# Kernel optimization log

Measured on AMD Instinct MI355X. Metric: run time of the kernel, lower is better.

Reference implementation:

```python
import jax, jax.numpy as jnp
import numpy as np

N_PEP, N_MHC, N_TCR = 20000, 5000, 100000
EMB, HID = 128, 256
E_PM, E_MT = 200000, 400000
B = 50000


def setup_inputs() -> dict:
    key = jax.random.key(0)
    ks = jax.random.split(key, 30)
    f32 = jnp.float32

    def w(k, shape, fan_in):
        # torch Linear default: U(-1/sqrt(fan_in), 1/sqrt(fan_in))
        lim = 1.0 / np.sqrt(fan_in)
        return jax.random.uniform(k, shape, dtype=f32, minval=-lim, maxval=lim)

    inp = {
        # embedding tables (learned params)
        "emb_pep": jax.random.normal(ks[0], (N_PEP, EMB), dtype=f32),
        "emb_mhc": jax.random.normal(ks[1], (N_MHC, EMB), dtype=f32),
        "emb_tcr": jax.random.normal(ks[2], (N_TCR, EMB), dtype=f32),
        # edge lists (src=edge_index[0], dst=edge_index[1])
        "src_pm": jax.random.randint(ks[3], (E_PM,), 0, N_PEP, dtype=jnp.int32),
        "dst_pm": jax.random.randint(ks[4], (E_PM,), 0, N_MHC, dtype=jnp.int32),
        "src_mt": jax.random.randint(ks[5], (E_MT,), 0, N_MHC, dtype=jnp.int32),
        "dst_mt": jax.random.randint(ks[6], (E_MT,), 0, N_TCR, dtype=jnp.int32),
        # triplet pack indices
        "pack_pep": jax.random.randint(ks[7], (B,), 0, N_PEP, dtype=jnp.int32),
        "pack_mhc": jax.random.randint(ks[8], (B,), 0, N_MHC, dtype=jnp.int32),
        "pack_tcr": jax.random.randint(ks[9], (B,), 0, N_TCR, dtype=jnp.int32),
        # SAGEConv params: Wl (aggregated neighbors, with bias), Wr (root, no bias)
        # layer 1: pep->mhc (src 128, dst 128); mhc->tcr (src 128, dst 128)
        "l1_pm_Wl": w(ks[10], (HID, EMB), EMB), "l1_pm_bl": w(ks[11], (HID,), EMB),
        "l1_pm_Wr": w(ks[12], (HID, EMB), EMB),
        "l1_mt_Wl": w(ks[13], (HID, EMB), EMB), "l1_mt_bl": w(ks[14], (HID,), EMB),
        "l1_mt_Wr": w(ks[15], (HID, EMB), EMB),
        # layer 2: pep->mhc (src 128, dst 256); mhc->tcr (src 256, dst 256)
        "l2_pm_Wl": w(ks[16], (HID, EMB), EMB), "l2_pm_bl": w(ks[17], (HID,), EMB),
        "l2_pm_Wr": w(ks[18], (HID, HID), HID),
        "l2_mt_Wl": w(ks[19], (HID, HID), HID), "l2_mt_bl": w(ks[20], (HID,), HID),
        "l2_mt_Wr": w(ks[21], (HID, HID), HID),
        # proj_pep and head MLP
        "proj_W": w(ks[22], (HID, EMB), EMB), "proj_b": w(ks[23], (HID,), EMB),
        "head_W1": w(ks[24], (HID, 3 * HID), 3 * HID), "head_b1": w(ks[25], (HID,), 3 * HID),
        "head_W2": w(ks[26], (1, HID), HID), "head_b2": w(ks[27], (1,), HID),
    }
    return inp


def _sage(x_src, x_dst, src, dst, Wl, bl, Wr, n_dst):
    # SAGEConv(mean): lin_l(mean_{j in N(i)} x_src[j]) + lin_r(x_dst[i])
    msg = jax.ops.segment_sum(x_src[src], dst, num_segments=n_dst)  # [n_dst, d_src]
    cnt = jax.ops.segment_sum(jnp.ones((src.shape[0],), x_src.dtype), dst, num_segments=n_dst)
    mean = msg / jnp.maximum(cnt, 1.0)[:, None]
    return mean @ Wl.T + bl + x_dst @ Wr.T


def reference(emb_pep, emb_mhc, emb_tcr,
              src_pm, dst_pm, src_mt, dst_mt,
              pack_pep, pack_mhc, pack_tcr,
              l1_pm_Wl, l1_pm_bl, l1_pm_Wr, l1_mt_Wl, l1_mt_bl, l1_mt_Wr,
              l2_pm_Wl, l2_pm_bl, l2_pm_Wr, l2_mt_Wl, l2_mt_bl, l2_mt_Wr,
              proj_W, proj_b, head_W1, head_b1, head_W2, head_b2):
    relu = jax.nn.relu
    # layer 1 (HeteroConv reads all relations from the same input dict)
    mhc1 = relu(_sage(emb_pep, emb_mhc, src_pm, dst_pm, l1_pm_Wl, l1_pm_bl, l1_pm_Wr, N_MHC))
    tcr1 = relu(_sage(emb_mhc, emb_tcr, src_mt, dst_mt, l1_mt_Wl, l1_mt_bl, l1_mt_Wr, N_TCR))
    # layer 2 ('pep' is never a destination, so it keeps its embedding)
    mhc2 = relu(_sage(emb_pep, mhc1, src_pm, dst_pm, l2_pm_Wl, l2_pm_bl, l2_pm_Wr, N_MHC))
    tcr2 = relu(_sage(mhc1, tcr1, src_mt, dst_mt, l2_mt_Wl, l2_mt_bl, l2_mt_Wr, N_TCR))
    # projections + triplet gather (dropout disabled: inference)
    hp = (emb_pep @ proj_W.T + proj_b)[pack_pep]  # [B, HID]
    hm = mhc2[pack_mhc]
    ht = tcr2[pack_tcr]
    z = jnp.concatenate([hp, hm, ht], axis=-1)  # [B, 3*HID]
    hidden = relu(z @ head_W1.T + head_b1)
    logits = hidden @ head_W2.T + head_b2
    return logits.squeeze(-1)
```

## Files before the change

kernel.cpp:

```cpp
#include <hip/hip_runtime.h>

constexpr int NPEP = 20000, NMHC = 5000, NTCR = 100000;
constexpr int EPM = 200000, EMT = 400000, BB = 50000;
constexpr int MAXU = 50000;

typedef __attribute__((ext_vector_type(8))) short bf16x8;
typedef __attribute__((ext_vector_type(4))) float f32x4;

__device__ inline ushort f2bf(float x) {
    union { float f; unsigned u; } v; v.f = x;
    unsigned r = (v.u + 0x7FFF + ((v.u >> 16) & 1)) >> 16;
    return (ushort)r;
}
__device__ inline float bf2f(ushort b) {
    union { unsigned u; float f; } t; t.u = ((unsigned)b) << 16; return t.f;
}
__device__ inline void bf2x2(unsigned u, float& a, float& b) {
    union { unsigned x; float f; } t1, t2;
    t1.x = u << 16; t2.x = u & 0xffff0000u;
    a = t1.f; b = t2.f;
}
__device__ inline ushort4 f4bf(float4 v) {
    return make_ushort4(f2bf(v.x), f2bf(v.y), f2bf(v.z), f2bf(v.w));
}

__global__ __launch_bounds__(256) void prep_kernel(
    int* __restrict__ ibz,
    const float4* __restrict__ emb_pep, ushort4* __restrict__ emb_pep_b,
    const float4* __restrict__ Wr1f, ushort4* __restrict__ Wr1_b,
    const float4* __restrict__ Wr2f, ushort4* __restrict__ Wr2_b,
    const float* __restrict__ head_W1, ushort4* __restrict__ W1b_b, ushort4* __restrict__ W1c_b,
    const float* __restrict__ l1_pm_Wl, const float* __restrict__ l1_pm_Wr,
    const float* __restrict__ l1_mt_Wl, ushort* __restrict__ Wcat1_b,
    const float* __restrict__ l2_pm_Wl, const float* __restrict__ l2_pm_Wr,
    const float* __restrict__ l2_mt_Wl, ushort* __restrict__ Wcat2_b,
    const float4* __restrict__ emb_mhc, ushort* __restrict__ Acat1,
    const float* __restrict__ proj_W, const float* __restrict__ proj_b,
    ushort* __restrict__ Wcomp_b, float* __restrict__ bp) {
    __shared__ float red[128];
    const int b = blockIdx.x, tid = threadIdx.x;
    if (b < 303) {
        int i = b * 256 + tid;
        if (i < 77500) ((int4*)ibz)[i] = make_int4(0, 0, 0, 0);
    } else if (b < 2803) {
        int i = (b - 303) * 256 + tid;
        if (i < 640000) emb_pep_b[i] = f4bf(emb_pep[i]);
    } else if (b < 2835) {
        int i = (b - 2803) * 256 + tid;
        if (i < 8192) Wr1_b[i] = f4bf(Wr1f[i]);
    } else if (b < 2899) {
        int i = (b - 2835) * 256 + tid;
        if (i < 16384) Wr2_b[i] = f4bf(Wr2f[i]);
    } else if (b < 2963) {
        int i = (b - 2899) * 256 + tid;
        if (i < 16384) {
            int n = i >> 6, k4 = (i & 63) * 4;
            float4 v = *(const float4*)(head_W1 + (size_t)n * 768 + 256 + k4);
            W1b_b[i] = f4bf(v);
        }
    } else if (b < 3027) {
        int i = (b - 2963) * 256 + tid;
        if (i < 16384) {
            int n = i >> 6, k4 = (i & 63) * 4;
            float4 v = *(const float4*)(head_W1 + (size_t)n * 768 + 512 + k4);
            W1c_b[i] = f4bf(v);
        }
    } else if (b < 3539) {
        int idx = (b - 3027) * 256 + tid;
        if (idx < 131072) {
            int r = idx >> 8, k = idx & 255;
            float v;
            if (r < 256) v = (k < 128) ? l1_pm_Wl[r * 128 + k] : l1_pm_Wr[r * 128 + (k - 128)];
            else         v = (k < 128) ? 0.f : l1_mt_Wl[(r - 256) * 128 + (k - 128)];
            Wcat1_b[idx] = f2bf(v);
        }
    } else if (b < 4307) {
        int idx = (b - 3539) * 256 + tid;
        if (idx < 196608) {
            int r = idx / 384, k = idx - r * 384;
            float v;
            if (r < 256) v = (k < 128) ? l2_pm_Wl[r * 128 + k] : l2_pm_Wr[r * 256 + (k - 128)];
            else         v = (k < 128) ? 0.f : l2_mt_Wl[(r - 256) * 256 + (k - 128)];
            Wcat2_b[idx] = f2bf(v);
        }
    } else if (b < 4932) {
        int i4 = (b - 4307) * 256 + tid;
        if (i4 < 160000) {
            int r = i4 >> 5, c4 = (i4 & 31) * 4;
            *(ushort4*)(Acat1 + (size_t)r * 256 + 128 + c4) = f4bf(emb_mhc[i4]);
        }
    } else {
        int i = b - 4932;
        const float* w1row = head_W1 + (size_t)i * 768;
        if (tid < 128) {
            float acc = 0.f;
            for (int k = 0; k < 256; k++) acc += w1row[k] * proj_W[k * 128 + tid];
            Wcomp_b[i * 128 + tid] = f2bf(acc);
            float pb = w1row[2 * tid] * proj_b[2 * tid] + w1row[2 * tid + 1] * proj_b[2 * tid + 1];
            red[tid] = pb;
        }
        __syncthreads();
        if (tid < 64) { red[tid] += red[tid + 64]; }
        __syncthreads();
        if (tid < 32) { red[tid] += red[tid + 32]; }
        __syncthreads();
        if (tid == 0) {
            float s = 0.f;
            for (int j = 0; j < 32; j++) s += red[j];
            bp[i] = s;
        }
    }
}

__global__ void hist2_kernel(const int* __restrict__ dst_pm, const int* __restrict__ dst_mt,
                             const int* __restrict__ pack_tcr,
                             int* __restrict__ deg_pm, int* __restrict__ deg_mt,
                             int* __restrict__ mark) {
    int t = blockIdx.x * blockDim.x + threadIdx.x;
    if (t < EPM) atomicAdd(&deg_pm[dst_pm[t]], 1);
    else if (t < EPM + EMT) atomicAdd(&deg_mt[dst_mt[t - EPM]], 1);
    else if (t < EPM + EMT + BB) mark[pack_tcr[t - EPM - EMT]] = 1;
}

__global__ __launch_bounds__(256) void blocksum2_kernel(const int* __restrict__ deg_pm,
                                                        const int* __restrict__ deg_mt,
                                                        const int* __restrict__ mark,
                                                        int* __restrict__ bsum_pm,
                                                        int* __restrict__ bsum_mt,
                                                        int* __restrict__ bsum_mk) {
    __shared__ int red[256];
    const int tid = threadIdx.x;
    const int* deg; int n, bi; int* bsum;
    if (blockIdx.x < 5) { deg = deg_pm; n = NMHC; bi = blockIdx.x; bsum = bsum_pm; }
    else if (blockIdx.x < 103) { deg = deg_mt; n = NTCR; bi = blockIdx.x - 5; bsum = bsum_mt; }
    else { deg = mark; n = NTCR; bi = blockIdx.x - 103; bsum = bsum_mk; }
    const int base = bi * 1024;
    int s = 0;
#pragma unroll
    for (int j = 0; j < 4; j++) {
        int i = base + tid + j * 256;
        if (i < n) s += deg[i];
    }
    red[tid] = s;
    __syncthreads();
    for (int off = 128; off > 0; off >>= 1) {
        if (tid < off) red[tid] += red[tid + off];
        __syncthreads();
    }
    if (tid == 0) bsum[bi] = red[0];
}

__global__ __launch_bounds__(128) void scanb2_kernel(int* __restrict__ bsum_pm,
                                                     int* __restrict__ bsum_mt,
                                                     int* __restrict__ bsum_mk) {
    __shared__ int s[128];
    const int tid = threadIdx.x;
    int* bsum = (blockIdx.x == 0) ? bsum_pm : ((blockIdx.x == 1) ? bsum_mt : bsum_mk);
    const int nb = (blockIdx.x == 0) ? 5 : 98;
    int v = (tid < nb) ? bsum[tid] : 0;
    s[tid] = v;
    __syncthreads();
    for (int off = 1; off < 128; off <<= 1) {
        int t = (tid >= off) ? s[tid - off] : 0;
        __syncthreads();
        s[tid] += t;
        __syncthreads();
    }
    if (tid < nb) bsum[tid] = (tid > 0) ? s[tid - 1] : 0;
    if (tid == 0) bsum[nb] = s[nb - 1];
}

__global__ __launch_bounds__(256) void emit2_kernel(const int* __restrict__ deg_pm,
                                                    const int* __restrict__ deg_mt,
                                                    const int* __restrict__ mark,
                                                    const int* __restrict__ bsum_pm,
                                                    const int* __restrict__ bsum_mt,
                                                    const int* __restrict__ bsum_mk,
                                                    int* __restrict__ rp_pm, float* __restrict__ cnt_pm,
                                                    int* __restrict__ rp_mt, float* __restrict__ cnt_mt,
                                                    int* __restrict__ list) {
    __shared__ int tsum[256];
    const int tid = threadIdx.x;
    const int* deg; const int* bsum; int* rp; float* cnt; int n, nb, bi, mode;
    if (blockIdx.x < 5) { deg = deg_pm; bsum = bsum_pm; rp = rp_pm; cnt = cnt_pm; n = NMHC; nb = 5; bi = blockIdx.x; mode = 0; }
    else if (blockIdx.x < 103) { deg = deg_mt; bsum = bsum_mt; rp = rp_mt; cnt = cnt_mt; n = NTCR; nb = 98; bi = blockIdx.x - 5; mode = 0; }
    else { deg = mark; bsum = bsum_mk; rp = nullptr; cnt = nullptr; n = NTCR; nb = 98; bi = blockIdx.x - 103; mode = 1; }
    const int i0 = bi * 1024 + tid * 4;
    int4 v = make_int4(0, 0, 0, 0);
    if (i0 + 3 < n) v = *(const int4*)(deg + i0);
    else if (i0 < n) {
        int t[4] = {0, 0, 0, 0};
        for (int j = 0; j < 4 && i0 + j < n; j++) t[j] = deg[i0 + j];
        v = make_int4(t[0], t[1], t[2], t[3]);
    }
    int s = v.x + v.y + v.z + v.w;
    tsum[tid] = s;
    __syncthreads();
    for (int off = 1; off < 256; off <<= 1) {
        int t = (tid >= off) ? tsum[tid - off] : 0;
        __syncthreads();
        tsum[tid] += t;
        __syncthreads();
    }
    int ex = ((tid > 0) ? tsum[tid - 1] : 0) + bsum[bi];
    if (mode == 0) {
        if (i0 + 3 < n) {
            int r1 = ex + v.x, r2 = r1 + v.y, r3 = r2 + v.z;
            *(int4*)(rp + i0) = make_int4(ex, r1, r2, r3);
            *(float4*)(cnt + i0) = make_float4((float)v.x, (float)v.y, (float)v.z, (float)v.w);
        } else if (i0 < n) {
            int r = ex;
            int vv[4] = {v.x, v.y, v.z, v.w};
            for (int j = 0; j < 4 && i0 + j < n; j++) {
                rp[i0 + j] = r;
                cnt[i0 + j] = (float)vv[j];
                r += vv[j];
            }
        }
        if (bi == 0 && tid == 0) rp[n] = bsum[nb];
    } else {
        int p = ex;
        int vv[4] = {v.x, v.y, v.z, v.w};
#pragma unroll
        for (int j = 0; j < 4; j++) {
            if (i0 + j < n && vv[j]) list[p++] = i0 + j;
        }
    }
}

__global__ void fill2_kernel(const int* __restrict__ src_pm, const int* __restrict__ dst_pm,
                             const int* __restrict__ src_mt, const int* __restrict__ dst_mt,
                             const int* __restrict__ rp_pm, int* __restrict__ cur_pm, int* __restrict__ csr_pm,
                             const int* __restrict__ rp_mt, int* __restrict__ cur_mt, int* __restrict__ csr_mt) {
    int t = blockIdx.x * blockDim.x + threadIdx.x;
    if (t < EPM) {
        int d = dst_pm[t];
        int pos = atomicAdd(&cur_pm[d], 1);
        csr_pm[rp_pm[d] + pos] = src_pm[t];
    } else if (t < EPM + EMT) {
        int t2 = t - EPM;
        int d = dst_mt[t2];
        int pos = atomicAdd(&cur_mt[d], 1);
        csr_mt[rp_mt[d] + pos] = src_mt[t2];
    }
}

__global__ __launch_bounds__(256) void gatherpm_kernel(const int* __restrict__ rp,
                                                       const int* __restrict__ csr_src,
                                                       const float* __restrict__ X,
                                                       ushort* __restrict__ A1, ushort* __restrict__ A2,
                                                       int n) {
    const int tid = threadIdx.x;
    const int r = blockIdx.x * 8 + (tid >> 5);
    const int lane = tid & 31;
    if (r >= n) return;
    const int e0 = rp[r], e1 = rp[r + 1];
    float4 s = make_float4(0.f, 0.f, 0.f, 0.f);
    for (int e = e0; e < e1; e++) {
        const int sidx = csr_src[e];
        float4 v = ((const float4*)(X + (long)sidx * 128))[lane];
        s.x += v.x; s.y += v.y; s.z += v.z; s.w += v.w;
    }
    float sc = 1.f / fmaxf((float)(e1 - e0), 1.f);
    ushort4 o = make_ushort4(f2bf(s.x * sc), f2bf(s.y * sc), f2bf(s.z * sc), f2bf(s.w * sc));
    *(ushort4*)(A1 + (size_t)r * 256 + lane * 4) = o;
    *(ushort4*)(A2 + (size_t)r * 384 + lane * 4) = o;
}

__global__ __launch_bounds__(256) void gatherb2_kernel(const int* __restrict__ rp,
                                                       const int* __restrict__ csr_src,
                                                       const ushort* __restrict__ Z1,
                                                       const ushort* __restrict__ Z2,
                                                       const int* __restrict__ list,
                                                       const int* __restrict__ nrowsp,
                                                       const float4* __restrict__ etc4,
                                                       ushort4* __restrict__ etc_bc,
                                                       float* __restrict__ cntc,
                                                       ushort* __restrict__ a1,
                                                       ushort* __restrict__ a2) {
    const int tid = threadIdx.x;
    const int r = blockIdx.x * 8 + (tid >> 5);
    const int lane = tid & 31;
    const int nrows = nrowsp[0];
    if (r >= nrows) return;
    const int orig = list[r];
    const int e0 = rp[orig], e1 = rp[orig + 1];
    float4 ev = etc4[(size_t)orig * 32 + lane];
    etc_bc[(size_t)r * 32 + lane] = f4bf(ev);
    if (lane == 0) cntc[r] = (float)(e1 - e0);
    float s1[8] = {}, s2[8] = {};
    for (int e = e0; e < e1; e++) {
        const int sidx = csr_src[e];
        uint4 u1 = *(const uint4*)(Z1 + (size_t)sidx * 256 + lane * 8);
        uint4 u2 = *(const uint4*)(Z2 + (size_t)sidx * 256 + lane * 8);
        float a, b;
        bf2x2(u1.x, a, b); s1[0] += a; s1[1] += b;
        bf2x2(u1.y, a, b); s1[2] += a; s1[3] += b;
        bf2x2(u1.z, a, b); s1[4] += a; s1[5] += b;
        bf2x2(u1.w, a, b); s1[6] += a; s1[7] += b;
        bf2x2(u2.x, a, b); s2[0] += a; s2[1] += b;
        bf2x2(u2.y, a, b); s2[2] += a; s2[3] += b;
        bf2x2(u2.z, a, b); s2[4] += a; s2[5] += b;
        bf2x2(u2.w, a, b); s2[6] += a; s2[7] += b;
    }
    uint4 w1, w2;
    w1.x = (unsigned)f2bf(s1[0]) | ((unsigned)f2bf(s1[1]) << 16);
    w1.y = (unsigned)f2bf(s1[2]) | ((unsigned)f2bf(s1[3]) << 16);
    w1.z = (unsigned)f2bf(s1[4]) | ((unsigned)f2bf(s1[5]) << 16);
    w1.w = (unsigned)f2bf(s1[6]) | ((unsigned)f2bf(s1[7]) << 16);
    w2.x = (unsigned)f2bf(s2[0]) | ((unsigned)f2bf(s2[1]) << 16);
    w2.y = (unsigned)f2bf(s2[2]) | ((unsigned)f2bf(s2[3]) << 16);
    w2.z = (unsigned)f2bf(s2[4]) | ((unsigned)f2bf(s2[5]) << 16);
    w2.w = (unsigned)f2bf(s2[6]) | ((unsigned)f2bf(s2[7]) << 16);
    *(uint4*)(a1 + (size_t)r * 256 + lane * 8) = w1;
    *(uint4*)(a2 + (size_t)r * 256 + lane * 8) = w2;
}

template <int K, int NB0, bool RELU0, bool G2>
__global__ __launch_bounds__(256, 2) void mfma_fused_kernel(
    int M, const ushort* __restrict__ A, const ushort* __restrict__ W,
    const float* __restrict__ bias,
    ushort* __restrict__ out0, int s0, ushort* __restrict__ out1) {
    constexpr int RS = 40;
    __shared__ ushort Als[128 * RS];
    __shared__ ushort Wls[128 * RS];
    const int tid = threadIdx.x;
    const int m0 = blockIdx.x * 128, n0 = blockIdx.y * 128;
    const int lane = tid & 63, w = tid >> 6;
    const int wm = w >> 1, wn = w & 1;
    const int m16 = lane & 15, q = lane >> 4;

    f32x4 acc[4][4] = {};

    for (int k0 = 0; k0 < K; k0 += 32) {
        bf16x8 a_st[2], w_st[2];
#pragma unroll
        for (int r = 0; r < 2; r++) {
            int chunk = tid + r * 256;
            int row = chunk >> 2, off = (chunk & 3) * 8;
            int ga = min(m0 + row, M - 1);
            a_st[r] = *(const bf16x8*)(A + (size_t)ga * K + k0 + off);
            w_st[r] = *(const bf16x8*)(W + (size_t)(n0 + row) * K + k0 + off);
        }
        __syncthreads();
#pragma unroll
        for (int r = 0; r < 2; r++) {
            int chunk = tid + r * 256;
            int row = chunk >> 2, off = (chunk & 3) * 8;
            *(bf16x8*)(&Als[row * RS + off]) = a_st[r];
            *(bf16x8*)(&Wls[row * RS + off]) = w_st[r];
        }
        __syncthreads();
        bf16x8 af[4], bf[4];
#pragma unroll
        for (int t = 0; t < 4; t++) {
            af[t] = *(const bf16x8*)(&Als[(wm * 64 + t * 16 + m16) * RS + q * 8]);
            bf[t] = *(const bf16x8*)(&Wls[(wn * 64 + t * 16 + m16) * RS + q * 8]);
        }
#pragma unroll
        for (int mt = 0; mt < 4; mt++)
#pragma unroll
            for (int nt = 0; nt < 4; nt++)
                acc[mt][nt] = __builtin_amdgcn_mfma_f32_16x16x32_bf16(af[mt], bf[nt], acc[mt][nt], 0, 0, 0);
    }

    const bool g1 = G2 && ((int)blockIdx.y >= NB0);
#pragma unroll
    for (int mt = 0; mt < 4; mt++) {
#pragma unroll
        for (int i = 0; i < 4; i++) {
            int row = m0 + wm * 64 + mt * 16 + q * 4 + i;
            if (row >= M) continue;
#pragma unroll
            for (int nt = 0; nt < 4; nt++) {
                int col = n0 + wn * 64 + nt * 16 + m16;
                float v = acc[mt][nt][i];
                if (!g1) {
                    v += bias[col];
                    if (RELU0) v = fmaxf(v, 0.f);
                    out0[(size_t)row * s0 + col] = f2bf(v);
                } else {
                    out1[(size_t)row * 256 + (col - NB0 * 128)] = f2bf(v);
                }
            }
        }
    }
}

template <int K>
__global__ __launch_bounds__(256, 2) void rowgemm_kernel(
    const int* __restrict__ nrowsp, const ushort* __restrict__ A, const ushort* __restrict__ W,
    const float* __restrict__ bias, const float* __restrict__ cnt,
    const ushort* __restrict__ accp, ushort* __restrict__ Cb) {
    constexpr int RS = 40;
    __shared__ ushort Als[128 * RS];
    __shared__ ushort Wls[256 * RS];
    const int tid = threadIdx.x;
    const int M = nrowsp[0];
    const int m0 = blockIdx.x * 128;
    if (m0 >= M) return;
    const int lane = tid & 63, w = tid >> 6;
    const int wm = w >> 1, wn = w & 1;
    const int m16 = lane & 15, q = lane >> 4;

    f32x4 acc[4][8] = {};

    for (int k0 = 0; k0 < K; k0 += 32) {
        bf16x8 a_st[2], w_st[4];
#pragma unroll
        for (int r = 0; r < 2; r++) {
            int chunk = tid + r * 256;
            int row = chunk >> 2, off = (chunk & 3) * 8;
            int ga = min(m0 + row, M - 1);
            a_st[r] = *(const bf16x8*)(A + (size_t)ga * K + k0 + off);
        }
#pragma unroll
        for (int r = 0; r < 4; r++) {
            int chunk = tid + r * 256;
            int row = chunk >> 2, off = (chunk & 3) * 8;
            w_st[r] = *(const bf16x8*)(W + (size_t)row * K + k0 + off);
        }
        __syncthreads();
#pragma unroll
        for (int r = 0; r < 2; r++) {
            int chunk = tid + r * 256;
            int row = chunk >> 2, off = (chunk & 3) * 8;
            *(bf16x8*)(&Als[row * RS + off]) = a_st[r];
        }
#pragma unroll
        for (int r = 0; r < 4; r++) {
            int chunk = tid + r * 256;
            int row = chunk >> 2, off = (chunk & 3) * 8;
            *(bf16x8*)(&Wls[row * RS + off]) = w_st[r];
        }
        __syncthreads();
        bf16x8 af[4], bf[8];
#pragma unroll
        for (int t = 0; t < 4; t++)
            af[t] = *(const bf16x8*)(&Als[(wm * 64 + t * 16 + m16) * RS + q * 8]);
#pragma unroll
        for (int t = 0; t < 8; t++)
            bf[t] = *(const bf16x8*)(&Wls[(wn * 128 + t * 16 + m16) * RS + q * 8]);
#pragma unroll
        for (int mt = 0; mt < 4; mt++)
#pragma unroll
            for (int nt = 0; nt < 8; nt++)
                acc[mt][nt] = __builtin_amdgcn_mfma_f32_16x16x32_bf16(af[mt], bf[nt], acc[mt][nt], 0, 0, 0);
    }

#pragma unroll
    for (int mt = 0; mt < 4; mt++) {
#pragma unroll
        for (int i = 0; i < 4; i++) {
            int row = m0 + wm * 64 + mt * 16 + q * 4 + i;
            if (row >= M) continue;
            float es = 1.f / fmaxf(cnt[row], 1.f);
#pragma unroll
            for (int nt = 0; nt < 8; nt++) {
                int col = wn * 128 + nt * 16 + m16;
                float v = acc[mt][nt][i] + bias[col] + bf2f(accp[(size_t)row * 256 + col]) * es;
                Cb[(size_t)row * 256 + col] = f2bf(fmaxf(v, 0.f));
            }
        }
    }
}

__global__ __launch_bounds__(256, 2) void tcr2ht_kernel(
    const int* __restrict__ nrowsp, const int* __restrict__ list,
    const ushort* __restrict__ T1, const ushort* __restrict__ Wr2,
    const ushort* __restrict__ W1c,
    const float* __restrict__ bl2, const float* __restrict__ cnt,
    const ushort* __restrict__ acc2, ushort* __restrict__ Ht) {
    constexpr int RS = 40;
    constexpr int RS2 = 264;
    __shared__ ushort Als[64 * RS];
    __shared__ ushort Wls[256 * RS];
    __shared__ ushort T[64 * RS2];
    const int tid = threadIdx.x;
    const int M = nrowsp[0];
    const int m0 = blockIdx.x * 64;
    if (m0 >= M) return;
    const int lane = tid & 63, w = tid >> 6;
    const int m16 = lane & 15, q = lane >> 4;

    {
        f32x4 acc[4][4] = {};
        for (int k0 = 0; k0 < 256; k0 += 32) {
            bf16x8 a_st, w_st[4];
            {
                int row = tid >> 2, off = (tid & 3) * 8;
                int ga = min(m0 + row, M - 1);
                a_st = *(const bf16x8*)(T1 + (size_t)ga * 256 + k0 + off);
            }
#pragma unroll
            for (int r = 0; r < 4; r++) {
                int chunk = tid + r * 256;
                int row = chunk >> 2, off = (chunk & 3) * 8;
                w_st[r] = *(const bf16x8*)(Wr2 + (size_t)row * 256 + k0 + off);
            }
            __syncthreads();
            {
                int row = tid >> 2, off = (tid & 3) * 8;
                *(bf16x8*)(&Als[row * RS + off]) = a_st;
            }
#pragma unroll
            for (int r = 0; r < 4; r++) {
                int chunk = tid + r * 256;
                int row = chunk >> 2, off = (chunk & 3) * 8;
                *(bf16x8*)(&Wls[row * RS + off]) = w_st[r];
            }
            __syncthreads();
            bf16x8 af[4], bf[4];
#pragma unroll
            for (int t = 0; t < 4; t++) {
                af[t] = *(const bf16x8*)(&Als[(t * 16 + m16) * RS + q * 8]);
                bf[t] = *(const bf16x8*)(&Wls[(w * 64 + t * 16 + m16) * RS + q * 8]);
            }
#pragma unroll
            for (int mt = 0; mt < 4; mt++)
#pragma unroll
                for (int nt = 0; nt < 4; nt++)
                    acc[mt][nt] = __builtin_amdgcn_mfma_f32_16x16x32_bf16(af[mt], bf[nt], acc[mt][nt], 0, 0, 0);
        }
#pragma unroll
        for (int mt = 0; mt < 4; mt++)
#pragma unroll
            for (int i = 0; i < 4; i++) {
                int lr = mt * 16 + q * 4 + i;
                int rc = min(m0 + lr, M - 1);
                float es = 1.f / fmaxf(cnt[rc], 1.f);
#pragma unroll
                for (int nt = 0; nt < 4; nt++) {
                    int col = w * 64 + nt * 16 + m16;
                    float v = acc[mt][nt][i] + bl2[col] + bf2f(acc2[(size_t)rc * 256 + col]) * es;
                    T[lr * RS2 + col] = f2bf(fmaxf(v, 0.f));
                }
            }
    }
    __syncthreads();

    {
        f32x4 acc[4][4] = {};
        for (int k0 = 0; k0 < 256; k0 += 32) {
            bf16x8 af[4], bf[4];
#pragma unroll
            for (int t = 0; t < 4; t++)
                af[t] = *(const bf16x8*)(&T[(t * 16 + m16) * RS2 + k0 + q * 8]);
#pragma unroll
            for (int t = 0; t < 4; t++) {
                int n = w * 64 + t * 16 + m16;
                bf[t] = *(const bf16x8*)(W1c + (size_t)n * 256 + k0 + q * 8);
            }
#pragma unroll
            for (int mt = 0; mt < 4; mt++)
#pragma unroll
                for (int nt = 0; nt < 4; nt++)
                    acc[mt][nt] = __builtin_amdgcn_mfma_f32_16x16x32_bf16(af[mt], bf[nt], acc[mt][nt], 0, 0, 0);
        }
#pragma unroll
        for (int mt = 0; mt < 4; mt++)
#pragma unroll
            for (int i = 0; i < 4; i++) {
                int row = m0 + mt * 16 + q * 4 + i;
                if (row >= M) continue;
                int orig = list[row];
#pragma unroll
                for (int nt = 0; nt < 4; nt++) {
                    int col = w * 64 + nt * 16 + m16;
                    Ht[(size_t)orig * 256 + col] = f2bf(acc[mt][nt][i]);
                }
            }
    }
}

template <int K, bool HASB>
__global__ __launch_bounds__(256, 2) void mfma_out_kernel(
    int M, const ushort* __restrict__ A, const ushort* __restrict__ W,
    const float* __restrict__ bias, ushort* __restrict__ out) {
    constexpr int RS = 40;
    __shared__ ushort Als[128 * RS];
    __shared__ ushort Wls[128 * RS];
    const int tid = threadIdx.x;
    const int m0 = blockIdx.x * 128, n0 = blockIdx.y * 128;
    const int lane = tid & 63, w = tid >> 6;
    const int wm = w >> 1, wn = w & 1;
    const int m16 = lane & 15, q = lane >> 4;

    f32x4 acc[4][4] = {};

    for (int k0 = 0; k0 < K; k0 += 32) {
        bf16x8 a_st[2], w_st[2];
#pragma unroll
        for (int r = 0; r < 2; r++) {
            int chunk = tid + r * 256;
            int row = chunk >> 2, off = (chunk & 3) * 8;
            int ga = min(m0 + row, M - 1);
            a_st[r] = *(const bf16x8*)(A + (size_t)ga * K + k0 + off);
            w_st[r] = *(const bf16x8*)(W + (size_t)(n0 + row) * K + k0 + off);
        }
        __syncthreads();
#pragma unroll
        for (int r = 0; r < 2; r++) {
            int chunk = tid + r * 256;
            int row = chunk >> 2, off = (chunk & 3) * 8;
            *(bf16x8*)(&Als[row * RS + off]) = a_st[r];
            *(bf16x8*)(&Wls[row * RS + off]) = w_st[r];
        }
        __syncthreads();
        bf16x8 af[4], bf[4];
#pragma unroll
        for (int t = 0; t < 4; t++) {
            af[t] = *(const bf16x8*)(&Als[(wm * 64 + t * 16 + m16) * RS + q * 8]);
            bf[t] = *(const bf16x8*)(&Wls[(wn * 64 + t * 16 + m16) * RS + q * 8]);
        }
#pragma unroll
        for (int mt = 0; mt < 4; mt++)
#pragma unroll
            for (int nt = 0; nt < 4; nt++)
                acc[mt][nt] = __builtin_amdgcn_mfma_f32_16x16x32_bf16(af[mt], bf[nt], acc[mt][nt], 0, 0, 0);
    }

#pragma unroll
    for (int mt = 0; mt < 4; mt++) {
#pragma unroll
        for (int i = 0; i < 4; i++) {
            int row = m0 + wm * 64 + mt * 16 + q * 4 + i;
            if (row >= M) continue;
#pragma unroll
            for (int nt = 0; nt < 4; nt++) {
                int col = n0 + wn * 64 + nt * 16 + m16;
                float v = acc[mt][nt][i];
                if (HASB) v += bias[col];
                out[(size_t)row * 256 + col] = f2bf(v);
            }
        }
    }
}

__global__ __launch_bounds__(256) void combine_kernel(
    const ushort* __restrict__ Hp, const ushort* __restrict__ Hm, const ushort* __restrict__ Ht,
    const int* __restrict__ pp, const int* __restrict__ pm, const int* __restrict__ pt,
    const float* __restrict__ b1, const float* __restrict__ W2, const float* __restrict__ b2,
    float* __restrict__ out) {
    const int tid = threadIdx.x;
    const int lane = tid & 63, w = tid >> 6;
    const int c = lane * 4;
    const float4 b1v = *(const float4*)(b1 + c);
    const float4 w2v = *(const float4*)(W2 + c);
    const float b2v = b2[0];
    const int base = blockIdx.x * 32 + w * 8;
#pragma unroll
    for (int t = 0; t < 8; t++) {
        int i = base + t;
        if (i >= BB) return;
        int ra = pp[i], rb = pm[i], rc = pt[i];
        ushort4 ua = *(const ushort4*)(Hp + (size_t)ra * 256 + c);
        ushort4 ub = *(const ushort4*)(Hm + (size_t)rb * 256 + c);
        ushort4 uc = *(const ushort4*)(Ht + (size_t)rc * 256 + c);
        float h0 = fmaxf(bf2f(ua.x) + bf2f(ub.x) + bf2f(uc.x) + b1v.x, 0.f);
        float h1 = fmaxf(bf2f(ua.y) + bf2f(ub.y) + bf2f(uc.y) + b1v.y, 0.f);
        float h2 = fmaxf(bf2f(ua.z) + bf2f(ub.z) + bf2f(uc.z) + b1v.z, 0.f);
        float h3 = fmaxf(bf2f(ua.w) + bf2f(ub.w) + bf2f(uc.w) + b1v.w, 0.f);
        float p = h0 * w2v.x + h1 * w2v.y + h2 * w2v.z + h3 * w2v.w;
#pragma unroll
        for (int off = 32; off > 0; off >>= 1) p += __shfl_down(p, off);
        if (lane == 0) out[i] = p + b2v;
    }
}

extern "C" void kernel_launch(void* const* d_in, const int* in_sizes, int n_in,
                              void* d_out, int out_size, void* d_ws, size_t ws_size,
                              hipStream_t stream) {
    const float* emb_pep = (const float*)d_in[0];
    const float* emb_mhc = (const float*)d_in[1];
    const float* emb_tcr = (const float*)d_in[2];
    const int* src_pm = (const int*)d_in[3];
    const int* dst_pm = (const int*)d_in[4];
    const int* src_mt = (const int*)d_in[5];
    const int* dst_mt = (const int*)d_in[6];
    const int* pack_pep = (const int*)d_in[7];
    const int* pack_mhc = (const int*)d_in[8];
    const int* pack_tcr = (const int*)d_in[9];
    const float* l1_pm_Wl = (const float*)d_in[10];
    const float* l1_pm_bl = (const float*)d_in[11];
    const float* l1_pm_Wr = (const float*)d_in[12];
    const float* l1_mt_Wl = (const float*)d_in[13];
    const float* l1_mt_bl = (const float*)d_in[14];
    const float* l1_mt_Wr = (const float*)d_in[15];
    const float* l2_pm_Wl = (const float*)d_in[16];
    const float* l2_pm_bl = (const float*)d_in[17];
    const float* l2_pm_Wr = (const float*)d_in[18];
    const float* l2_mt_Wl = (const float*)d_in[19];
    const float* l2_mt_bl = (const float*)d_in[20];
    const float* l2_mt_Wr = (const float*)d_in[21];
    const float* proj_W = (const float*)d_in[22];
    const float* proj_b = (const float*)d_in[23];
    const float* head_W1 = (const float*)d_in[24];
    const float* head_b1 = (const float*)d_in[25];
    const float* head_W2 = (const float*)d_in[26];
    const float* head_b2 = (const float*)d_in[27];
    float* out = (float*)d_out;

    int* ib = (int*)d_ws;
    int* deg_pm = ib;
    int* cur_pm = ib + 5000;
    int* deg_mt = ib + 10000;
    int* cur_mt = ib + 110000;
    int* mark   = ib + 210000;
    int* rp_pm  = ib + 310000;
    int* rp_mt  = ib + 315008;
    int* csr_pm = ib + 415016;
    int* csr_mt = ib + 615016;
    int* bsum_pm = ib + 1015016;
    int* bsum_mt = ib + 1015176;
    int* bsum_mk = ib + 1015336;
    int* list    = ib + 1015496;

    float* f = (float*)(ib + 1065544);
    float* cnt_pm = f;
    float* cnt_mt = f + 5000;
    float* cntc   = f + 105000;
    float* bp     = f + 155000;

    ushort* u = (ushort*)(f + 155264);
    ushort* Wcat1_b = u;
    ushort* Wcat2_b = u + 131072;
    ushort* W1b_b   = u + 327680;
    ushort* W1c_b   = u + 393216;
    ushort* Wcomp_b = u + 458752;
    ushort* Wr1_b   = u + 491520;
    ushort* Wr2_b   = u + 524288;
    ushort* Acat1   = u + 589824;
    ushort* Acat2   = u + 1869824;
    ushort* Zb1     = u + 3789824;
    ushort* Zb2     = u + 5069824;
    ushort* mhc2_b  = u + 6349824;
    ushort* emb_pep_b = u + 7629824;
    ushort* Hp_b    = u + 10189824;
    ushort* Hm_b    = u + 15309824;
    ushort* etc_bc  = u + 16589824;
    ushort* acc1_c  = u + 22989824;
    ushort* tcr1_c  = u + 35789824;
    ushort* acc2_c  = u + 48589824;
    ushort* Ht_b    = u + 61389824;

    prep_kernel<<<5188, 256, 0, stream>>>(
        ib,
        (const float4*)emb_pep, (ushort4*)emb_pep_b,
        (const float4*)l1_mt_Wr, (ushort4*)Wr1_b,
        (const float4*)l2_mt_Wr, (ushort4*)Wr2_b,
        head_W1, (ushort4*)W1b_b, (ushort4*)W1c_b,
        l1_pm_Wl, l1_pm_Wr, l1_mt_Wl, Wcat1_b,
        l2_pm_Wl, l2_pm_Wr, l2_mt_Wl, Wcat2_b,
        (const float4*)emb_mhc, Acat1,
        proj_W, proj_b, Wcomp_b, bp);

    hist2_kernel<<<(EPM + EMT + BB + 255) / 256, 256, 0, stream>>>(
        dst_pm, dst_mt, pack_tcr, deg_pm, deg_mt, mark);
    blocksum2_kernel<<<201, 256, 0, stream>>>(deg_pm, deg_mt, mark, bsum_pm, bsum_mt, bsum_mk);
    scanb2_kernel<<<3, 128, 0, stream>>>(bsum_pm, bsum_mt, bsum_mk);
    emit2_kernel<<<201, 256, 0, stream>>>(deg_pm, deg_mt, mark, bsum_pm, bsum_mt, bsum_mk,
                                          rp_pm, cnt_pm, rp_mt, cnt_mt, list);
    fill2_kernel<<<(EPM + EMT + 255) / 256, 256, 0, stream>>>(
        src_pm, dst_pm, src_mt, dst_mt, rp_pm, cur_pm, csr_pm, rp_mt, cur_mt, csr_mt);

    gatherpm_kernel<<<(NMHC + 7) / 8, 256, 0, stream>>>(rp_pm, csr_pm, emb_pep, Acat1, Acat2, NMHC);

    mfma_fused_kernel<256, 2, true, true><<<dim3((NMHC + 127) / 128, 4), 256, 0, stream>>>(
        NMHC, Acat1, Wcat1_b, l1_pm_bl, Acat2 + 128, 384, Zb1);
    mfma_fused_kernel<384, 2, true, true><<<dim3((NMHC + 127) / 128, 4), 256, 0, stream>>>(
        NMHC, Acat2, Wcat2_b, l2_pm_bl, mhc2_b, 256, Zb2);

    gatherb2_kernel<<<(MAXU + 7) / 8, 256, 0, stream>>>(
        rp_mt, csr_mt, Zb1, Zb2, list, bsum_mk + 98,
        (const float4*)emb_tcr, (ushort4*)etc_bc, cntc, acc1_c, acc2_c);

    rowgemm_kernel<128><<<(MAXU + 127) / 128, 256, 0, stream>>>(
        bsum_mk + 98, etc_bc, Wr1_b, l1_mt_bl, cntc, acc1_c, tcr1_c);

    tcr2ht_kernel<<<(MAXU + 63) / 64, 256, 0, stream>>>(
        bsum_mk + 98, list, tcr1_c, Wr2_b, W1c_b, l2_mt_bl, cntc, acc2_c, Ht_b);

    mfma_out_kernel<128, true><<<dim3((NPEP + 127) / 128, 2), 256, 0, stream>>>(
        NPEP, emb_pep_b, Wcomp_b, bp, Hp_b);
    mfma_out_kernel<256, false><<<dim3((NMHC + 127) / 128, 2), 256, 0, stream>>>(
        NMHC, mhc2_b, W1b_b, nullptr, Hm_b);

    combine_kernel<<<(BB + 31) / 32, 256, 0, stream>>>(
        Hp_b, Hm_b, Ht_b, pack_pep, pack_mhc, pack_tcr,
        head_b1, head_W2, head_b2, out);
}
```

Before: 416.0 us.

## Fuse TCR layer-1, layer-2 and head GEMMs into one kernel with smem intermediates

Result: slower. 436.7 us (+5.0%).

```diff
diff --git a/kernel.cpp b/kernel.cpp
--- a/kernel.cpp
+++ b/kernel.cpp
@@ -273,8 +273,6 @@
                                                        const ushort* __restrict__ Z2,
                                                        const int* __restrict__ list,
                                                        const int* __restrict__ nrowsp,
-                                                       const float4* __restrict__ etc4,
-                                                       ushort4* __restrict__ etc_bc,
                                                        float* __restrict__ cntc,
                                                        ushort* __restrict__ a1,
                                                        ushort* __restrict__ a2) {
@@ -285,8 +283,6 @@
     if (r >= nrows) return;
     const int orig = list[r];
     const int e0 = rp[orig], e1 = rp[orig + 1];
-    float4 ev = etc4[(size_t)orig * 32 + lane];
-    etc_bc[(size_t)r * 32 + lane] = f4bf(ev);
     if (lane == 0) cntc[r] = (float)(e1 - e0);
     float s1[8] = {}, s2[8] = {};
     for (int e = e0; e < e1; e++) {
@@ -387,95 +383,18 @@
     }
 }
 
-template <int K>
-__global__ __launch_bounds__(256, 2) void rowgemm_kernel(
-    const int* __restrict__ nrowsp, const ushort* __restrict__ A, const ushort* __restrict__ W,
-    const float* __restrict__ bias, const float* __restrict__ cnt,
-    const ushort* __restrict__ accp, ushort* __restrict__ Cb) {
-    constexpr int RS = 40;
-    __shared__ ushort Als[128 * RS];
-    __shared__ ushort Wls[256 * RS];
-    const int tid = threadIdx.x;
-    const int M = nrowsp[0];
-    const int m0 = blockIdx.x * 128;
-    if (m0 >= M) return;
-    const int lane = tid & 63, w = tid >> 6;
-    const int wm = w >> 1, wn = w & 1;
-    const int m16 = lane & 15, q = lane >> 4;
-
-    f32x4 acc[4][8] = {};
-
-    for (int k0 = 0; k0 < K; k0 += 32) {
-        bf16x8 a_st[2], w_st[4];
-#pragma unroll
-        for (int r = 0; r < 2; r++) {
-            int chunk = tid + r * 256;
-            int row = chunk >> 2, off = (chunk & 3) * 8;
-            int ga = min(m0 + row, M - 1);
-            a_st[r] = *(const bf16x8*)(A + (size_t)ga * K + k0 + off);
-        }
-#pragma unroll
-        for (int r = 0; r < 4; r++) {
-            int chunk = tid + r * 256;
-            int row = chunk >> 2, off = (chunk & 3) * 8;
-            w_st[r] = *(const bf16x8*)(W + (size_t)row * K + k0 + off);
-        }
-        __syncthreads();
-#pragma unroll
-        for (int r = 0; r < 2; r++) {
-            int chunk = tid + r * 256;
-            int row = chunk >> 2, off = (chunk & 3) * 8;
-            *(bf16x8*)(&Als[row * RS + off]) = a_st[r];
-        }
-#pragma unroll
-        for (int r = 0; r < 4; r++) {
-            int chunk = tid + r * 256;
-            int row = chunk >> 2, off = (chunk & 3) * 8;
-            *(bf16x8*)(&Wls[row * RS + off]) = w_st[r];
-        }
-        __syncthreads();
-        bf16x8 af[4], bf[8];
-#pragma unroll
-        for (int t = 0; t < 4; t++)
-            af[t] = *(const bf16x8*)(&Als[(wm * 64 + t * 16 + m16) * RS + q * 8]);
-#pragma unroll
-        for (int t = 0; t < 8; t++)
-            bf[t] = *(const bf16x8*)(&Wls[(wn * 128 + t * 16 + m16) * RS + q * 8]);
-#pragma unroll
-        for (int mt = 0; mt < 4; mt++)
-#pragma unroll
-            for (int nt = 0; nt < 8; nt++)
-                acc[mt][nt] = __builtin_amdgcn_mfma_f32_16x16x32_bf16(af[mt], bf[nt], acc[mt][nt], 0, 0, 0);
-    }
-
-#pragma unroll
-    for (int mt = 0; mt < 4; mt++) {
-#pragma unroll
-        for (int i = 0; i < 4; i++) {
-            int row = m0 + wm * 64 + mt * 16 + q * 4 + i;
-            if (row >= M) continue;
-            float es = 1.f / fmaxf(cnt[row], 1.f);
-#pragma unroll
-            for (int nt = 0; nt < 8; nt++) {
-                int col = wn * 128 + nt * 16 + m16;
-                float v = acc[mt][nt][i] + bias[col] + bf2f(accp[(size_t)row * 256 + col]) * es;
-                Cb[(size_t)row * 256 + col] = f2bf(fmaxf(v, 0.f));
-            }
-        }
-    }
-}
-
-__global__ __launch_bounds__(256, 2) void tcr2ht_kernel(
+__global__ __launch_bounds__(256, 4) void tcrall_kernel(
     const int* __restrict__ nrowsp, const int* __restrict__ list,
-    const ushort* __restrict__ T1, const ushort* __restrict__ Wr2,
+    const float* __restrict__ emb_tcr,
+    const ushort* __restrict__ Wr1, const ushort* __restrict__ Wr2,
     const ushort* __restrict__ W1c,
-    const float* __restrict__ bl2, const float* __restrict__ cnt,
-    const ushort* __restrict__ acc2, ushort* __restrict__ Ht) {
-    constexpr int RS = 40;
+    const float* __restrict__ bl1, const float* __restrict__ bl2,
+    const float* __restrict__ cnt,
+    const ushort* __restrict__ acc1, const ushort* __restrict__ acc2,
+    ushort* __restrict__ Ht) {
+    constexpr int RS1 = 136;
     constexpr int RS2 = 264;
-    __shared__ ushort Als[64 * RS];
-    __shared__ ushort Wls[256 * RS];
-    __shared__ ushort T[64 * RS2];
+    __shared__ ushort B[64 * RS2];
     const int tid = threadIdx.x;
     const int M = nrowsp[0];
     const int m0 = blockIdx.x * 64;
@@ -483,38 +402,24 @@
     const int lane = tid & 63, w = tid >> 6;
     const int m16 = lane & 15, q = lane >> 4;
 
+#pragma unroll
+    for (int r = 0; r < 8; r++) {
+        int chunk = tid + r * 256;
+        int row = chunk >> 5, c4 = (chunk & 31) * 4;
+        int grow = list[min(m0 + row, M - 1)];
+        float4 v = *(const float4*)(emb_tcr + (size_t)grow * 128 + c4);
+        *(ushort4*)(&B[row * RS1 + c4]) = f4bf(v);
+    }
+    __syncthreads();
+
     {
         f32x4 acc[4][4] = {};
-        for (int k0 = 0; k0 < 256; k0 += 32) {
-            bf16x8 a_st, w_st[4];
-            {
-                int row = tid >> 2, off = (tid & 3) * 8;
-                int ga = min(m0 + row, M - 1);
-                a_st = *(const bf16x8*)(T1 + (size_t)ga * 256 + k0 + off);
-            }
-#pragma unroll
-            for (int r = 0; r < 4; r++) {
-                int chunk = tid + r * 256;
-                int row = chunk >> 2, off = (chunk & 3) * 8;
-                w_st[r] = *(const bf16x8*)(Wr2 + (size_t)row * 256 + k0 + off);
-            }
-            __syncthreads();
-            {
-                int row = tid >> 2, off = (tid & 3) * 8;
-                *(bf16x8*)(&Als[row * RS + off]) = a_st;
-            }
-#pragma unroll
-            for (int r = 0; r < 4; r++) {
-                int chunk = tid + r * 256;
-                int row = chunk >> 2, off = (chunk & 3) * 8;
-                *(bf16x8*)(&Wls[row * RS + off]) = w_st[r];
-            }
-            __syncthreads();
+        for (int k0 = 0; k0 < 128; k0 += 32) {
             bf16x8 af[4], bf[4];
 #pragma unroll
             for (int t = 0; t < 4; t++) {
-                af[t] = *(const bf16x8*)(&Als[(t * 16 + m16) * RS + q * 8]);
-                bf[t] = *(const bf16x8*)(&Wls[(w * 64 + t * 16 + m16) * RS + q * 8]);
+                af[t] = *(const bf16x8*)(&B[(t * 16 + m16) * RS1 + k0 + q * 8]);
+                bf[t] = *(const bf16x8*)(Wr1 + (size_t)(w * 64 + t * 16 + m16) * 128 + k0 + q * 8);
             }
 #pragma unroll
             for (int mt = 0; mt < 4; mt++)
@@ -522,6 +427,7 @@
                 for (int nt = 0; nt < 4; nt++)
                     acc[mt][nt] = __builtin_amdgcn_mfma_f32_16x16x32_bf16(af[mt], bf[nt], acc[mt][nt], 0, 0, 0);
         }
+        __syncthreads();
 #pragma unroll
         for (int mt = 0; mt < 4; mt++)
 #pragma unroll
@@ -532,8 +438,8 @@
 #pragma unroll
                 for (int nt = 0; nt < 4; nt++) {
                     int col = w * 64 + nt * 16 + m16;
-                    float v = acc[mt][nt][i] + bl2[col] + bf2f(acc2[(size_t)rc * 256 + col]) * es;
-                    T[lr * RS2 + col] = f2bf(fmaxf(v, 0.f));
+                    float v = acc[mt][nt][i] + bl1[col] + bf2f(acc1[(size_t)rc * 256 + col]) * es;
+                    B[lr * RS2 + col] = f2bf(fmaxf(v, 0.f));
                 }
             }
     }
@@ -544,12 +450,42 @@
         for (int k0 = 0; k0 < 256; k0 += 32) {
             bf16x8 af[4], bf[4];
 #pragma unroll
-            for (int t = 0; t < 4; t++)
-                af[t] = *(const bf16x8*)(&T[(t * 16 + m16) * RS2 + k0 + q * 8]);
-#pragma unroll
             for (int t = 0; t < 4; t++) {
-                int n = w * 64 + t * 16 + m16;
-                bf[t] = *(const bf16x8*)(W1c + (size_t)n * 256 + k0 + q * 8);
+                af[t] = *(const bf16x8*)(&B[(t * 16 + m16) * RS2 + k0 + q * 8]);
+                bf[t] = *(const bf16x8*)(Wr2 + (size_t)(w * 64 + t * 16 + m16) * 256 + k0 + q * 8);
+            }
+#pragma unroll
+            for (int mt = 0; mt < 4; mt++)
+#pragma unroll
+                for (int nt = 0; nt < 4; nt++)
+                    acc[mt][nt] = __builtin_amdgcn_mfma_f32_16x16x32_bf16(af[mt], bf[nt], acc[mt][nt], 0, 0, 0);
+        }
+        __syncthreads();
+#pragma unroll
+        for (int mt = 0; mt < 4; mt++)
+#pragma unroll
+            for (int i = 0; i < 4; i++) {
+                int lr = mt * 16 + q * 4 + i;
+                int rc = min(m0 + lr, M - 1);
+                float es = 1.f / fmaxf(cnt[rc], 1.f);
+#pragma unroll
+                for (int nt = 0; nt < 4; nt++) {
+                    int col = w * 64 + nt * 16 + m16;
+                    float v = acc[mt][nt][i] + bl2[col] + bf2f(acc2[(size_t)rc * 256 + col]) * es;
+                    B[lr * RS2 + col] = f2bf(fmaxf(v, 0.f));
+                }
+            }
+    }
+    __syncthreads();
+
+    {
+        f32x4 acc[4][4] = {};
+        for (int k0 = 0; k0 < 256; k0 += 32) {
+            bf16x8 af[4], bf[4];
+#pragma unroll
+            for (int t = 0; t < 4; t++) {
+                af[t] = *(const bf16x8*)(&B[(t * 16 + m16) * RS2 + k0 + q * 8]);
+                bf[t] = *(const bf16x8*)(W1c + (size_t)(w * 64 + t * 16 + m16) * 256 + k0 + q * 8);
             }
 #pragma unroll
             for (int mt = 0; mt < 4; mt++)
@@ -738,11 +674,9 @@
     ushort* emb_pep_b = u + 7629824;
     ushort* Hp_b    = u + 10189824;
     ushort* Hm_b    = u + 15309824;
-    ushort* etc_bc  = u + 16589824;
-    ushort* acc1_c  = u + 22989824;
-    ushort* tcr1_c  = u + 35789824;
-    ushort* acc2_c  = u + 48589824;
-    ushort* Ht_b    = u + 61389824;
+    ushort* acc1_c  = u + 16589824;
+    ushort* acc2_c  = u + 29389824;
+    ushort* Ht_b    = u + 42189824;
 
     prep_kernel<<<5188, 256, 0, stream>>>(
         ib,
@@ -772,14 +706,11 @@
         NMHC, Acat2, Wcat2_b, l2_pm_bl, mhc2_b, 256, Zb2);
 
     gatherb2_kernel<<<(MAXU + 7) / 8, 256, 0, stream>>>(
-        rp_mt, csr_mt, Zb1, Zb2, list, bsum_mk + 98,
-        (const float4*)emb_tcr, (ushort4*)etc_bc, cntc, acc1_c, acc2_c);
-
-    rowgemm_kernel<128><<<(MAXU + 127) / 128, 256, 0, stream>>>(
-        bsum_mk + 98, etc_bc, Wr1_b, l1_mt_bl, cntc, acc1_c, tcr1_c);
-
-    tcr2ht_kernel<<<(MAXU + 63) / 64, 256, 0, stream>>>(
-        bsum_mk + 98, list, tcr1_c, Wr2_b, W1c_b, l2_mt_bl, cntc, acc2_c, Ht_b);
+        rp_mt, csr_mt, Zb1, Zb2, list, bsum_mk + 98, cntc, acc1_c, acc2_c);
+
+    tcrall_kernel<<<(MAXU + 63) / 64, 256, 0, stream>>>(
+        bsum_mk + 98, list, emb_tcr, Wr1_b, Wr2_b, W1c_b,
+        l1_mt_bl, l2_mt_bl, cntc, acc1_c, acc2_c, Ht_b);
 
     mfma_out_kernel<128, true><<<dim3((NPEP + 127) / 128, 2), 256, 0, stream>>>(
         NPEP, emb_pep_b, Wcomp_b, bp, Hp_b);
```
